# Performance work log

Measured on AMD Instinct MI355X. Metric: run time of the kernel, lower is better.

The kernel has to match this reference:

```python
import jax, jax.numpy as jnp
import numpy as np

D = 1024

def setup_inputs() -> dict:
    key = jax.random.key(0)
    k1, k2, k3, k4 = jax.random.split(key, 4)
    context = jax.random.normal(k1, (32, 2048, D), dtype=jnp.float32)
    # nn.Linear(dim, dim, bias=False): weight [D, D], applied as x @ W.T
    W = jax.random.normal(k2, (D, D), dtype=jnp.float32) / np.sqrt(D)
    # nn.Linear(dim, 1): weight [1, D], bias [1]
    v = jax.random.normal(k3, (D,), dtype=jnp.float32) / np.sqrt(D)
    b = jax.random.normal(k4, (), dtype=jnp.float32) * 0.01
    return {"context": context, "W": W, "v": v, "b": b}

def reference(context, W, v, b):
    # context: [B, S, D]
    h = jnp.tanh(jnp.einsum('bsd,ed->bse', context, W))      # [B, S, D]
    attn_logits = jnp.einsum('bsd,d->bs', h, v) + b          # [B, S]
    attn = jax.nn.softmax(attn_logits, axis=-1)              # softmax over sourceL
    weighted_context = jnp.einsum('bs,bsd->bd', attn, context)
    return weighted_context, attn
```

## Files before the change

### kernel.cpp

```cpp
#include <hip/hip_runtime.h>
#include <stdint.h>

#define BDIM 32
#define SDIM 2048
#define DDIM 1024
#define MDIM (BDIM * SDIM)

typedef __bf16 bf16x8 __attribute__((ext_vector_type(8)));
typedef float  f32x4  __attribute__((ext_vector_type(4)));


__device__ inline unsigned short f2bf(float f) {
  union { float f; unsigned u; } un; un.f = f;
  unsigned r = un.u + 0x7fffu + ((un.u >> 16) & 1u);
  return (unsigned short)(r >> 16);
}

__device__ inline float fast_tanh(float x) {
  float e = __expf(2.0f * x);
  return 1.0f - 2.0f / (e + 1.0f);
}

__device__ inline void gl_lds16(const unsigned short* g, unsigned short* l) {
  __builtin_amdgcn_global_load_lds(
      (__attribute__((address_space(1))) unsigned int*)(void*)(uintptr_t)g,
      (__attribute__((address_space(3))) unsigned int*)l,
      16, 0, 0);
}


__global__ __launch_bounds__(256) void cvt_kernel(const float* __restrict__ src,
                                                  unsigned short* __restrict__ dst) {
  size_t i = (size_t)blockIdx.x * 256 + threadIdx.x;
  const float4* s4 = (const float4*)src;
  float4 a = s4[2 * i];
  float4 b = s4[2 * i + 1];
  uint4 o;
  o.x = (unsigned)f2bf(a.x) | ((unsigned)f2bf(a.y) << 16);
  o.y = (unsigned)f2bf(a.z) | ((unsigned)f2bf(a.w) << 16);
  o.z = (unsigned)f2bf(b.x) | ((unsigned)f2bf(b.y) << 16);
  o.w = (unsigned)f2bf(b.z) | ((unsigned)f2bf(b.w) << 16);
  ((uint4*)dst)[i] = o;
}


__global__ __launch_bounds__(256) void gemm_logits(
    const unsigned short* __restrict__ A,
    const unsigned short* __restrict__ Bw,
    const float* __restrict__ v,
    float* __restrict__ logits)
{
  __shared__ __align__(16) unsigned short Al[128 * 64];
  __shared__ __align__(16) unsigned short Bl[128 * 64];

  const int t  = threadIdx.x;
  const int mt = blockIdx.x >> 3;
  const int nt = blockIdx.x & 7;
  const int m0 = mt * 128;
  const int n0 = nt * 128;
  const int w    = t >> 6;
  const int lane = t & 63;
  const int wm = (w >> 1) * 64;
  const int wn = (w & 1) * 64;
  const int c = lane & 15;
  const int q = lane >> 4;

  float vv[4];
#pragma unroll
  for (int ni = 0; ni < 4; ++ni) vv[ni] = v[n0 + wn + ni * 16 + c];

  f32x4 acc[4][4] = {};

  const int srow = t >> 3;
  const int scc  = ((t & 7) ^ (srow & 7)) * 8;
  const unsigned short* gA[4];
  const unsigned short* gB[4];
  unsigned short* lA[4];
  unsigned short* lB[4];
#pragma unroll
  for (int p = 0; p < 4; ++p) {
    gA[p] = A  + (size_t)(m0 + p * 32 + srow) * DDIM + scc;
    gB[p] = Bw + (size_t)(n0 + p * 32 + srow) * DDIM + scc;
    lA[p] = Al + p * 2048 + w * 512;
    lB[p] = Bl + p * 2048 + w * 512;
  }

  const int xr = c & 7;
  int arow[4], brow[4], koff[2];
#pragma unroll
  for (int mi = 0; mi < 4; ++mi) arow[mi] = (wm + mi * 16 + c) * 64;
#pragma unroll
  for (int ni = 0; ni < 4; ++ni) brow[ni] = (wn + ni * 16 + c) * 64;
#pragma unroll
  for (int ks = 0; ks < 2; ++ks) koff[ks] = ((ks * 4 + q) ^ xr) * 8;

  for (int kt = 0; kt < 16; ++kt) {
    const int k0 = kt * 64;
#pragma unroll
    for (int p = 0; p < 4; ++p) {
      gl_lds16(gA[p] + k0, lA[p]);
      gl_lds16(gB[p] + k0, lB[p]);
    }
    __syncthreads();

#pragma unroll
    for (int ks = 0; ks < 2; ++ks) {
      bf16x8 af[4], bfr[4];
#pragma unroll
      for (int mi = 0; mi < 4; ++mi)
        af[mi] = *(const bf16x8*)&Al[arow[mi] + koff[ks]];
#pragma unroll
      for (int ni = 0; ni < 4; ++ni)
        bfr[ni] = *(const bf16x8*)&Bl[brow[ni] + koff[ks]];

#pragma unroll
      for (int mi = 0; mi < 4; ++mi)
#pragma unroll
        for (int ni = 0; ni < 4; ++ni)
          acc[mi][ni] = __builtin_amdgcn_mfma_f32_16x16x32_bf16(
              af[mi], bfr[ni], acc[mi][ni], 0, 0, 0);
    }

    __syncthreads();
  }

#pragma unroll
  for (int mi = 0; mi < 4; ++mi) {
    float p0 = 0.f, p1 = 0.f, p2 = 0.f, p3 = 0.f;
#pragma unroll
    for (int ni = 0; ni < 4; ++ni) {
      const float vvn = vv[ni];
      p0 += fast_tanh(acc[mi][ni][0]) * vvn;
      p1 += fast_tanh(acc[mi][ni][1]) * vvn;
      p2 += fast_tanh(acc[mi][ni][2]) * vvn;
      p3 += fast_tanh(acc[mi][ni][3]) * vvn;
    }
#pragma unroll
    for (int mask = 1; mask <= 8; mask <<= 1) {
      p0 += __shfl_xor(p0, mask);
      p1 += __shfl_xor(p1, mask);
      p2 += __shfl_xor(p2, mask);
      p3 += __shfl_xor(p3, mask);
    }
    if (c == 0) {
      float* lp = logits + (m0 + wm + mi * 16 + q * 4);
      atomicAdd(lp + 0, p0);
      atomicAdd(lp + 1, p1);
      atomicAdd(lp + 2, p2);
      atomicAdd(lp + 3, p3);
    }
  }
}


__global__ __launch_bounds__(256) void softmax_kernel(float* __restrict__ la) {
  const int b = blockIdx.x;
  const int t = threadIdx.x;
  float* p = la + (size_t)b * SDIM;
  float x[8];
#pragma unroll
  for (int i = 0; i < 8; ++i) x[i] = p[i * 256 + t];
  float m = x[0];
#pragma unroll
  for (int i = 1; i < 8; ++i) m = fmaxf(m, x[i]);
#pragma unroll
  for (int mask = 1; mask < 64; mask <<= 1) m = fmaxf(m, __shfl_xor(m, mask));
  __shared__ float redm[4], reds[4];
  const int w = t >> 6, lane = t & 63;
  if (lane == 0) redm[w] = m;
  __syncthreads();
  m = fmaxf(fmaxf(redm[0], redm[1]), fmaxf(redm[2], redm[3]));
  float e[8];
  float s = 0.f;
#pragma unroll
  for (int i = 0; i < 8; ++i) { e[i] = __expf(x[i] - m); s += e[i]; }
#pragma unroll
  for (int mask = 1; mask < 64; mask <<= 1) s += __shfl_xor(s, mask);
  if (lane == 0) reds[w] = s;
  __syncthreads();
  s = reds[0] + reds[1] + reds[2] + reds[3];
  const float inv = 1.0f / s;
#pragma unroll
  for (int i = 0; i < 8; ++i) p[i * 256 + t] = e[i] * inv;
}


__global__ __launch_bounds__(256) void wsum_kernel(const float* __restrict__ ctx,
                                                   const float* __restrict__ attn,
                                                   float* __restrict__ wc) {
  const int b  = blockIdx.x >> 5;
  const int sc = blockIdx.x & 31;
  const int t  = threadIdx.x;
  __shared__ float as_[64];
  if (t < 64) as_[t] = attn[(size_t)b * SDIM + sc * 64 + t];
  __syncthreads();
  const float* cp = ctx + ((size_t)b * SDIM + sc * 64) * DDIM + t * 4;
  float4 a0 = {0.f, 0.f, 0.f, 0.f}, a1 = a0, a2 = a0, a3 = a0;
#pragma unroll 4
  for (int s = 0; s < 64; s += 4) {
    const float4 c0 = *(const float4*)(cp + (size_t)(s + 0) * DDIM);
    const float4 c1 = *(const float4*)(cp + (size_t)(s + 1) * DDIM);
    const float4 c2 = *(const float4*)(cp + (size_t)(s + 2) * DDIM);
    const float4 c3 = *(const float4*)(cp + (size_t)(s + 3) * DDIM);
    const float w0 = as_[s], w1 = as_[s + 1], w2 = as_[s + 2], w3 = as_[s + 3];
    a0.x += w0 * c0.x; a0.y += w0 * c0.y; a0.z += w0 * c0.z; a0.w += w0 * c0.w;
    a1.x += w1 * c1.x; a1.y += w1 * c1.y; a1.z += w1 * c1.z; a1.w += w1 * c1.w;
    a2.x += w2 * c2.x; a2.y += w2 * c2.y; a2.z += w2 * c2.z; a2.w += w2 * c2.w;
    a3.x += w3 * c3.x; a3.y += w3 * c3.y; a3.z += w3 * c3.z; a3.w += w3 * c3.w;
  }
  a0.x += a1.x + a2.x + a3.x;
  a0.y += a1.y + a2.y + a3.y;
  a0.z += a1.z + a2.z + a3.z;
  a0.w += a1.w + a2.w + a3.w;
  float* o = wc + (size_t)b * DDIM + t * 4;
  atomicAdd(o + 0, a0.x);
  atomicAdd(o + 1, a0.y);
  atomicAdd(o + 2, a0.z);
  atomicAdd(o + 3, a0.w);
}


extern "C" void kernel_launch(void* const* d_in, const int* in_sizes, int n_in,
                              void* d_out, int out_size, void* d_ws, size_t ws_size,
                              hipStream_t stream) {
  const float* ctx = (const float*)d_in[0];
  const float* W   = (const float*)d_in[1];
  const float* v   = (const float*)d_in[2];

  float* out_wc   = (float*)d_out;
  float* out_attn = out_wc + BDIM * DDIM;

  unsigned short* ctx_bf = (unsigned short*)d_ws;
  unsigned short* W_bf   = ctx_bf + (size_t)MDIM * DDIM;

  hipMemsetAsync(d_out, 0, (size_t)out_size * sizeof(float), stream);

  cvt_kernel<<<(MDIM * DDIM) / (256 * 8), 256, 0, stream>>>(ctx, ctx_bf);
  cvt_kernel<<<(DDIM * DDIM) / (256 * 8), 256, 0, stream>>>(W, W_bf);
  gemm_logits<<<(MDIM / 128) * (DDIM / 128), 256, 0, stream>>>(ctx_bf, W_bf, v, out_attn);
  softmax_kernel<<<BDIM, 256, 0, stream>>>(out_attn);
  wsum_kernel<<<BDIM * 32, 256, 0, stream>>>(ctx, out_attn, out_wc);
}
```

Before: 634.9 us.

## Loop all N-tiles inside one GEMM block and drop logit atomics

Each block now owns a 128-row M tile and iterates over all eight N tiles of W, accumulating the tanh·v partial logits in registers. The logits are reduced across the two N-warp halves in shared memory and written directly, which removes the global atomicAdds and shrinks the memset to only the weighted-context output. The K step drops from 64 to 32 with a new XOR swizzle, which halves LDS use but doubles the number of barrier pairs per tile. The grid is 8x smaller (512 blocks), which may hurt occupancy and load balance on a large GPU, and the A tile is re-read from L2 for every N tile.

Result: slower. 660.7 us (+4.1%).

```diff
diff --git a/kernel.cpp b/kernel.cpp
--- a/kernel.cpp
+++ b/kernel.cpp
@@ -50,14 +50,12 @@
     const float* __restrict__ v,
     float* __restrict__ logits)
 {
-  __shared__ __align__(16) unsigned short Al[128 * 64];
-  __shared__ __align__(16) unsigned short Bl[128 * 64];
+  __shared__ __align__(16) unsigned short Al[128 * 32];
+  __shared__ __align__(16) unsigned short Bl[128 * 32];
+  __shared__ float lred[2][128];
 
   const int t  = threadIdx.x;
-  const int mt = blockIdx.x >> 3;
-  const int nt = blockIdx.x & 7;
-  const int m0 = mt * 128;
-  const int n0 = nt * 128;
+  const int m0 = blockIdx.x * 128;
   const int w    = t >> 6;
   const int lane = t & 63;
   const int wm = (w >> 1) * 64;
@@ -65,53 +63,48 @@
   const int c = lane & 15;
   const int q = lane >> 4;
 
-  float vv[4];
-#pragma unroll
-  for (int ni = 0; ni < 4; ++ni) vv[ni] = v[n0 + wn + ni * 16 + c];
-
-  f32x4 acc[4][4] = {};
-
-  const int srow = t >> 3;
-  const int scc  = ((t & 7) ^ (srow & 7)) * 8;
-  const unsigned short* gA[4];
-  const unsigned short* gB[4];
-  unsigned short* lA[4];
-  unsigned short* lB[4];
-#pragma unroll
-  for (int p = 0; p < 4; ++p) {
-    gA[p] = A  + (size_t)(m0 + p * 32 + srow) * DDIM + scc;
-    gB[p] = Bw + (size_t)(n0 + p * 32 + srow) * DDIM + scc;
-    lA[p] = Al + p * 2048 + w * 512;
-    lB[p] = Bl + p * 2048 + w * 512;
-  }
-
-  const int xr = c & 7;
-  int arow[4], brow[4], koff[2];
-#pragma unroll
-  for (int mi = 0; mi < 4; ++mi) arow[mi] = (wm + mi * 16 + c) * 64;
-#pragma unroll
-  for (int ni = 0; ni < 4; ++ni) brow[ni] = (wn + ni * 16 + c) * 64;
-#pragma unroll
-  for (int ks = 0; ks < 2; ++ks) koff[ks] = ((ks * 4 + q) ^ xr) * 8;
-
-  for (int kt = 0; kt < 16; ++kt) {
-    const int k0 = kt * 64;
-#pragma unroll
-    for (int p = 0; p < 4; ++p) {
-      gl_lds16(gA[p] + k0, lA[p]);
-      gl_lds16(gB[p] + k0, lB[p]);
-    }
-    __syncthreads();
-
-#pragma unroll
-    for (int ks = 0; ks < 2; ++ks) {
+  const int srow = w * 16 + (lane >> 2);
+  const int cl   = ((lane & 3) ^ ((lane >> 2) & 3) ^ ((lane >> 4) & 3)) * 8;
+
+  const unsigned short* gA0 = A + (size_t)(m0 + srow) * DDIM + cl;
+  const unsigned short* gA1 = A + (size_t)(m0 + 64 + srow) * DDIM + cl;
+  unsigned short* lA0 = Al + (w * 16) * 32;
+  unsigned short* lA1 = Al + (64 + w * 16) * 32;
+  unsigned short* lB0 = Bl + (w * 16) * 32;
+  unsigned short* lB1 = Bl + (64 + w * 16) * 32;
+
+  const int xk = (q ^ (c & 3) ^ ((c >> 2) & 3)) * 8;
+  int arow[4], brow[4];
+#pragma unroll
+  for (int mi = 0; mi < 4; ++mi) arow[mi] = (wm + mi * 16 + c) * 32 + xk;
+#pragma unroll
+  for (int ni = 0; ni < 4; ++ni) brow[ni] = (wn + ni * 16 + c) * 32 + xk;
+
+  float lp[4][4] = {};
+
+  for (int nt = 0; nt < 8; ++nt) {
+    const int n0 = nt * 128;
+    float vv[4];
+#pragma unroll
+    for (int ni = 0; ni < 4; ++ni) vv[ni] = v[n0 + wn + ni * 16 + c];
+    const unsigned short* gB0 = Bw + (size_t)(n0 + srow) * DDIM + cl;
+    const unsigned short* gB1 = Bw + (size_t)(n0 + 64 + srow) * DDIM + cl;
+
+    f32x4 acc[4][4] = {};
+
+    for (int kt = 0; kt < 32; ++kt) {
+      const int k0 = kt * 32;
+      gl_lds16(gA0 + k0, lA0);
+      gl_lds16(gA1 + k0, lA1);
+      gl_lds16(gB0 + k0, lB0);
+      gl_lds16(gB1 + k0, lB1);
+      __syncthreads();
+
       bf16x8 af[4], bfr[4];
 #pragma unroll
-      for (int mi = 0; mi < 4; ++mi)
-        af[mi] = *(const bf16x8*)&Al[arow[mi] + koff[ks]];
-#pragma unroll
-      for (int ni = 0; ni < 4; ++ni)
-        bfr[ni] = *(const bf16x8*)&Bl[brow[ni] + koff[ks]];
+      for (int mi = 0; mi < 4; ++mi) af[mi] = *(const bf16x8*)&Al[arow[mi]];
+#pragma unroll
+      for (int ni = 0; ni < 4; ++ni) bfr[ni] = *(const bf16x8*)&Bl[brow[ni]];
 
 #pragma unroll
       for (int mi = 0; mi < 4; ++mi)
@@ -119,37 +112,39 @@
         for (int ni = 0; ni < 4; ++ni)
           acc[mi][ni] = __builtin_amdgcn_mfma_f32_16x16x32_bf16(
               af[mi], bfr[ni], acc[mi][ni], 0, 0, 0);
+
+      __syncthreads();
     }
 
-    __syncthreads();
+#pragma unroll
+    for (int mi = 0; mi < 4; ++mi)
+#pragma unroll
+      for (int r = 0; r < 4; ++r) {
+        float s = 0.f;
+#pragma unroll
+        for (int ni = 0; ni < 4; ++ni)
+          s += fast_tanh(acc[mi][ni][r]) * vv[ni];
+        lp[mi][r] += s;
+      }
   }
 
 #pragma unroll
-  for (int mi = 0; mi < 4; ++mi) {
-    float p0 = 0.f, p1 = 0.f, p2 = 0.f, p3 = 0.f;
-#pragma unroll
-    for (int ni = 0; ni < 4; ++ni) {
-      const float vvn = vv[ni];
-      p0 += fast_tanh(acc[mi][ni][0]) * vvn;
-      p1 += fast_tanh(acc[mi][ni][1]) * vvn;
-      p2 += fast_tanh(acc[mi][ni][2]) * vvn;
-      p3 += fast_tanh(acc[mi][ni][3]) * vvn;
+  for (int mi = 0; mi < 4; ++mi)
+#pragma unroll
+    for (int r = 0; r < 4; ++r) {
+#pragma unroll
+      for (int mask = 1; mask <= 8; mask <<= 1)
+        lp[mi][r] += __shfl_xor(lp[mi][r], mask);
     }
-#pragma unroll
-    for (int mask = 1; mask <= 8; mask <<= 1) {
-      p0 += __shfl_xor(p0, mask);
-      p1 += __shfl_xor(p1, mask);
-      p2 += __shfl_xor(p2, mask);
-      p3 += __shfl_xor(p3, mask);
-    }
-    if (c == 0) {
-      float* lp = logits + (m0 + wm + mi * 16 + q * 4);
-      atomicAdd(lp + 0, p0);
-      atomicAdd(lp + 1, p1);
-      atomicAdd(lp + 2, p2);
-      atomicAdd(lp + 3, p3);
-    }
+  if (c == 0) {
+#pragma unroll
+    for (int mi = 0; mi < 4; ++mi)
+#pragma unroll
+      for (int r = 0; r < 4; ++r)
+        lred[w & 1][wm + mi * 16 + q * 4 + r] = lp[mi][r];
   }
+  __syncthreads();
+  if (t < 128) logits[m0 + t] = lred[0][t] + lred[1][t];
 }
 
 
@@ -233,11 +228,11 @@
   unsigned short* ctx_bf = (unsigned short*)d_ws;
   unsigned short* W_bf   = ctx_bf + (size_t)MDIM * DDIM;
 
-  hipMemsetAsync(d_out, 0, (size_t)out_size * sizeof(float), stream);
+  hipMemsetAsync(out_wc, 0, (size_t)BDIM * DDIM * sizeof(float), stream);
 
   cvt_kernel<<<(MDIM * DDIM) / (256 * 8), 256, 0, stream>>>(ctx, ctx_bf);
   cvt_kernel<<<(DDIM * DDIM) / (256 * 8), 256, 0, stream>>>(W, W_bf);
-  gemm_logits<<<(MDIM / 128) * (DDIM / 128), 256, 0, stream>>>(ctx_bf, W_bf, v, out_attn);
+  gemm_logits<<<MDIM / 128, 256, 0, stream>>>(ctx_bf, W_bf, v, out_attn);
   softmax_kernel<<<BDIM, 256, 0, stream>>>(out_attn);
   wsum_kernel<<<BDIM * 32, 256, 0, stream>>>(ctx, out_attn, out_wc);
 }
```
